# Optimization experiments

Hardware: AMD Instinct MI355X
Metric: run time of the kernel (lower is better)

Reference implementation:

```python
import jax, jax.numpy as jnp
import numpy as np

NUM_TOKENS = 4096
LATENT_DIM = 256
BETA = 0.25
TEMPERATURE = 1.0  # temp_init buffer value
EPS_TEMP = 1e-6


def setup_inputs() -> dict:
    key = jax.random.key(0)
    k1, k2 = jax.random.split(key)
    latent = jax.random.normal(k1, (4, 2048, LATENT_DIM), dtype=jnp.float32)
    cb = jax.random.normal(k2, (NUM_TOKENS, LATENT_DIM), dtype=jnp.float32)
    # module normalizes codebook rows at init
    codebook = cb / jnp.linalg.norm(cb, axis=-1, keepdims=True)
    return {"latent": latent, "codebook": codebook}


def _l2norm(x):
    return x / jnp.clip(jnp.linalg.norm(x, axis=-1, keepdims=True), 1e-12)


def reference(latent, codebook):
    B, S, D = latent.shape
    flat = latent.reshape(-1, D)                       # [N, D]
    # cosine similarity via normalized matmul
    ln = _l2norm(flat)
    cn = _l2norm(codebook)
    cosine_sim = jnp.einsum('nd,kd->nk', ln, cn)       # [N, K]
    distances = 2.0 - 2.0 * cosine_sim
    scaled = distances / jnp.maximum(TEMPERATURE, EPS_TEMP)
    soft_assign = jax.nn.softmax(-scaled, axis=-1)     # [N, K]
    indices = jnp.argmax(soft_assign, axis=-1)         # [N]
    hard_assign = jax.nn.one_hot(indices, NUM_TOKENS, dtype=jnp.float32)
    # straight-through soft->hard assignment
    assign = hard_assign + soft_assign - jax.lax.stop_gradient(soft_assign)

    selected_cosine_sim = jnp.take_along_axis(cosine_sim, indices[:, None], axis=1).mean()

    # codebook pairwise euclidean diagnostics (off-diagonal mean / min)
    sq = jnp.sum(codebook * codebook, axis=-1)         # [K]
    d2 = sq[:, None] + sq[None, :] - 2.0 * (codebook @ codebook.T)
    cdist = jnp.sqrt(jnp.clip(d2, 0.0))                # [K, K]
    K = NUM_TOKENS
    off_sum = jnp.sum(cdist) - jnp.sum(jnp.diagonal(cdist))
    avg_euclidean = off_sum / (K * (K - 1))
    eye = jnp.eye(K, dtype=bool)
    min_euclidean = jnp.min(jnp.where(eye, jnp.inf, cdist))

    quantized = (assign @ codebook).reshape(B, S, D)
    commitment_loss = BETA * jnp.mean((jax.lax.stop_gradient(latent) - quantized) ** 2)
    codebook_loss = jnp.mean((latent - jax.lax.stop_gradient(quantized)) ** 2)
    quantized = latent + jax.lax.stop_gradient(quantized - latent)

    avg_probs = jnp.mean(hard_assign, axis=0)
    perplexity = jnp.exp(-jnp.sum(avg_probs * jnp.log(avg_probs + 1e-10)))

    return (quantized, indices, commitment_loss, codebook_loss, perplexity,
            selected_cosine_sim, avg_euclidean, min_euclidean)
```

## Files before the change

### kernel.cpp

```cpp
#include <hip/hip_runtime.h>
#include <hip/hip_bf16.h>
#include <math.h>

#define NTOK 8192
#define DIM 256
#define KCB 4096
#define NCB (KCB / 128)
#define NKEY 4
#define NKROW (NCB * NKEY)
#define DELTA 0.08f
#define GTIE 2e-6
#define MAXC 16
#define NPAIRB (NCB * (NCB + 1) / 2)

typedef unsigned long long ull;
typedef unsigned short ushort;
typedef __attribute__((ext_vector_type(8))) short shortx8;
typedef __attribute__((ext_vector_type(4))) float floatx4;
typedef const __attribute__((address_space(1))) void* gas_cp;
typedef __attribute__((address_space(3))) void* las_p;

__device__ __forceinline__ unsigned f2ord(float f) {
    unsigned u = __float_as_uint(f);
    return (u & 0x80000000u) ? ~u : (u | 0x80000000u);
}
__device__ __forceinline__ float ord2f(unsigned u) {
    unsigned b = (u & 0x80000000u) ? (u & 0x7FFFFFFFu) : ~u;
    return __uint_as_float(b);
}
__device__ __forceinline__ ushort f2bf(float f) {
    unsigned u = __float_as_uint(f);
    unsigned r = u + 0x7FFFu + ((u >> 16) & 1u);
    return (ushort)(r >> 16);
}

union TileSmem {
    struct { ushort a[128][64]; ushort b[128][64]; } t;
    unsigned keys[128][40];
};

__device__ __forceinline__ void stage_tile(const ushort* __restrict__ gbase,
                                           ushort (*lds)[64], int wave, int lane,
                                           int kk) {
    int p = lane & 7;
    int rsub = lane >> 3;
    int kc = p ^ (rsub & 7);
#pragma unroll
    for (int c = 0; c < 4; ++c) {
        int j = wave * 4 + c;
        const ushort* src = gbase + (size_t)(j * 8 + rsub) * DIM + kk + kc * 8;
        __builtin_amdgcn_global_load_lds((gas_cp)src, (las_p)&lds[j * 8][0], 16, 0, 0);
    }
}
__device__ __forceinline__ shortx8 frag_read(const ushort (*lds)[64], int row,
                                             int lc) {
    return *(const shortx8*)&lds[row][(lc ^ (row & 7)) * 8];
}

__device__ __forceinline__ float np_combine(const float* racc) {
    float h0 = __fadd_rn(__fadd_rn(__fadd_rn(racc[0], racc[1]), __fadd_rn(racc[2], racc[3])),
                         __fadd_rn(__fadd_rn(racc[4], racc[5]), __fadd_rn(racc[6], racc[7])));
    float h1 = __fadd_rn(__fadd_rn(__fadd_rn(racc[8], racc[9]), __fadd_rn(racc[10], racc[11])),
                         __fadd_rn(__fadd_rn(racc[12], racc[13]), __fadd_rn(racc[14], racc[15])));
    float s = __fadd_rn(h0, h1);
    return fmaxf(sqrtf(s), 1e-12f);
}

__global__ __launch_bounds__(256) void prep(const float* __restrict__ lat,
                                            const float* __restrict__ cb,
                                            float* __restrict__ nrml,
                                            float* __restrict__ nrmc,
                                            ushort* __restrict__ latbf,
                                            ushort* __restrict__ cnbf,
                                            ushort* __restrict__ cbbf,
                                            float* __restrict__ sq,
                                            unsigned* __restrict__ counts) {
    int bid = blockIdx.x, t = threadIdx.x;
    if (bid < NTOK) {
        int n = bid;
        if (n < KCB / 256) counts[n * 256 + t] = 0u;
        const float* row = lat + (size_t)n * DIM;
        latbf[(size_t)n * DIM + t] = f2bf(row[t]);
        __shared__ float racc[16];
        if (t < 16) {
            int h = t >> 3, j = t & 7;
            const float* p = row + h * 128;
            float r = __fmul_rn(p[j], p[j]);
#pragma unroll 1
            for (int i = 8; i < 128; i += 8)
                r = __fadd_rn(r, __fmul_rn(p[i + j], p[i + j]));
            racc[t] = r;
        }
        __syncthreads();
        if (t == 0) nrml[n] = np_combine(racc);
    } else {
        int n = bid - NTOK;
        __shared__ float racc2[16];
        __shared__ double dacc[16];
        __shared__ float snrm;
        const float* row = cb + (size_t)n * DIM;
        if (t < 16) {
            int h = t >> 3, j = t & 7;
            const float* p = row + h * 128;
            float r = __fmul_rn(p[j], p[j]);
            double ds = 0.0;
#pragma unroll 1
            for (int i = 8; i < 128; i += 8)
                r = __fadd_rn(r, __fmul_rn(p[i + j], p[i + j]));
#pragma unroll 1
            for (int i = 0; i < 128; i += 8) { double v = (double)p[i + j]; ds += v * v; }
            racc2[t] = r; dacc[t] = ds;
        }
        __syncthreads();
        if (t == 0) {
            float nr = np_combine(racc2);
            snrm = nr; nrmc[n] = nr;
            double ds = 0.0;
            for (int i = 0; i < 16; ++i) ds += dacc[i];
            sq[n] = (float)ds;
        }
        __syncthreads();
        float c = row[t];
        cnbf[(size_t)n * DIM + t] = f2bf(c / snrm);
        cbbf[(size_t)n * DIM + t] = f2bf(c);
    }
}

__global__ __launch_bounds__(256) void scores_mfma(const ushort* __restrict__ A,
                                                   const ushort* __restrict__ B,
                                                   unsigned* __restrict__ keysw) {
    __shared__ TileSmem sm;
    int tid = threadIdx.x;
    int wave = tid >> 6, lane = tid & 63;
    int quad = lane >> 4, l15 = lane & 15;
    int rowBase = blockIdx.y * 128, colBase = blockIdx.x * 128;
    int wrow = wave * 32;
    floatx4 acc[2][8];
#pragma unroll
    for (int m = 0; m < 2; ++m)
#pragma unroll
        for (int n = 0; n < 8; ++n) acc[m][n] = (floatx4){0.f, 0.f, 0.f, 0.f};
    const ushort* gA = A + (size_t)rowBase * DIM;
    const ushort* gB = B + (size_t)colBase * DIM;
#pragma unroll 1
    for (int kk = 0; kk < DIM; kk += 64) {
        __syncthreads();
        stage_tile(gA, sm.t.a, wave, lane, kk);
        stage_tile(gB, sm.t.b, wave, lane, kk);
        __syncthreads();
#pragma unroll
        for (int s = 0; s < 2; ++s) {
            shortx8 af[2], bf[8];
#pragma unroll
            for (int mt = 0; mt < 2; ++mt)
                af[mt] = frag_read(sm.t.a, wrow + mt * 16 + l15, s * 4 + quad);
#pragma unroll
            for (int nt = 0; nt < 8; ++nt)
                bf[nt] = frag_read(sm.t.b, nt * 16 + l15, s * 4 + quad);
#pragma unroll
            for (int mt = 0; mt < 2; ++mt)
#pragma unroll
                for (int nt = 0; nt < 8; ++nt)
                    acc[mt][nt] = __builtin_amdgcn_mfma_f32_16x16x32_bf16(
                        af[mt], bf[nt], acc[mt][nt], 0, 0, 0);
        }
    }
    __syncthreads();
    unsigned colp[8];
#pragma unroll
    for (int nt = 0; nt < 8; ++nt)
        colp[nt] = 4095u - (unsigned)(colBase + nt * 16 + l15);
#pragma unroll
    for (int mt = 0; mt < 2; ++mt)
#pragma unroll
        for (int reg = 0; reg < 4; ++reg) {
            unsigned b1 = 0u, b2 = 0u;
#pragma unroll
            for (int nt = 0; nt < 8; ++nt) {
                unsigned key = (f2ord(acc[mt][nt][reg]) & 0xFFFFF000u) | colp[nt];
                unsigned lo = min(key, b1);
                b1 = max(key, b1);
                b2 = max(lo, b2);
            }
            int row = wrow + mt * 16 + quad * 4 + reg;
            uint2 kv; kv.x = b1; kv.y = b2;
            *(uint2*)&sm.keys[row][l15 * 2] = kv;
        }
    __syncthreads();
    if (tid < 128) {
        unsigned a0 = 0, a1 = 0, a2 = 0, a3 = 0;
#pragma unroll
        for (int j = 0; j < 8; ++j) {
            uint4 v4 = *(const uint4*)&sm.keys[tid][j * 4];
            unsigned vs[4] = {v4.x, v4.y, v4.z, v4.w};
#pragma unroll
            for (int q = 0; q < 4; ++q) {
                unsigned v = vs[q];
                unsigned n0 = min(v, a0); a0 = max(v, a0);
                unsigned n1 = min(n0, a1); a1 = max(n0, a1);
                unsigned n2 = min(n1, a2); a2 = max(n1, a2);
                a3 = max(n2, a3);
            }
        }
        size_t base = (size_t)(rowBase + tid) * NKROW + blockIdx.x * NKEY;
        uint4 o; o.x = a0; o.y = a1; o.z = a2; o.w = a3;
        *(uint4*)&keysw[base] = o;
    }
}

__global__ __launch_bounds__(256) void pairwise_mfma(const ushort* __restrict__ C,
                                                     const float* __restrict__ sq,
                                                     float* __restrict__ psumw,
                                                     unsigned* __restrict__ pminw) {
    int tri = blockIdx.x;
    int a = (int)((sqrtf(8.f * tri + 1.f) - 1.f) * 0.5f);
    while ((a + 1) * (a + 2) / 2 <= tri) ++a;
    while (a * (a + 1) / 2 > tri) --a;
    int b = tri - a * (a + 1) / 2;
    int rowBase = b * 128, colBase = a * 128;
    __shared__ TileSmem sm;
    __shared__ float rs[256], rm[256];
    int tid = threadIdx.x;
    int wave = tid >> 6, lane = tid & 63;
    int quad = lane >> 4, l15 = lane & 15;
    int wrow = wave * 32;
    floatx4 acc[2][8];
#pragma unroll
    for (int m = 0; m < 2; ++m)
#pragma unroll
        for (int n = 0; n < 8; ++n) acc[m][n] = (floatx4){0.f, 0.f, 0.f, 0.f};
    const ushort* gA = C + (size_t)rowBase * DIM;
    const ushort* gB = C + (size_t)colBase * DIM;
#pragma unroll 1
    for (int kk = 0; kk < DIM; kk += 64) {
        __syncthreads();
        stage_tile(gA, sm.t.a, wave, lane, kk);
        stage_tile(gB, sm.t.b, wave, lane, kk);
        __syncthreads();
#pragma unroll
        for (int s = 0; s < 2; ++s) {
            shortx8 af[2], bf[8];
#pragma unroll
            for (int mt = 0; mt < 2; ++mt)
                af[mt] = frag_read(sm.t.a, wrow + mt * 16 + l15, s * 4 + quad);
#pragma unroll
            for (int nt = 0; nt < 8; ++nt)
                bf[nt] = frag_read(sm.t.b, nt * 16 + l15, s * 4 + quad);
#pragma unroll
            for (int mt = 0; mt < 2; ++mt)
#pragma unroll
                for (int nt = 0; nt < 8; ++nt)
                    acc[mt][nt] = __builtin_amdgcn_mfma_f32_16x16x32_bf16(
                        af[mt], bf[nt], acc[mt][nt], 0, 0, 0);
        }
    }
    float lsum = 0.f, lmin = INFINITY;
#pragma unroll
    for (int mt = 0; mt < 2; ++mt)
#pragma unroll
        for (int reg = 0; reg < 4; ++reg) {
            int i = rowBase + wrow + mt * 16 + quad * 4 + reg;
            float sqi = sq[i];
#pragma unroll
            for (int nt = 0; nt < 8; ++nt) {
                int j = colBase + nt * 16 + l15;
                float d2 = sqi + sq[j] - 2.0f * acc[mt][nt][reg];
                float d = sqrtf(fmaxf(d2, 0.0f));
                bool use = i < j;
                lsum += use ? d : 0.f;
                lmin = fminf(lmin, use ? d : INFINITY);
            }
        }
    rs[tid] = lsum; rm[tid] = lmin; __syncthreads();
    for (int s = 128; s > 0; s >>= 1) {
        if (tid < s) { rs[tid] += rs[tid + s]; rm[tid] = fminf(rm[tid], rm[tid + s]); }
        __syncthreads();
    }
    if (tid == 0) { psumw[tri] = rs[0]; pminw[tri] = f2ord(rm[0]); }
}

__global__ __launch_bounds__(256) void argmax_resolve(const float* __restrict__ lat,
                                                      const float* __restrict__ cb,
                                                      const float* __restrict__ nrml,
                                                      const float* __restrict__ nrmc,
                                                      const unsigned* __restrict__ keysw,
                                                      float* __restrict__ outidx,
                                                      float* __restrict__ outq,
                                                      unsigned* __restrict__ counts,
                                                      float* __restrict__ selw,
                                                      float* __restrict__ msew) {
    __shared__ int scand[4][MAXC];
    __shared__ double sc64[4][MAXC];
    int wid = threadIdx.x >> 6, lane = threadIdx.x & 63;
    int n = blockIdx.x * 4 + wid;
    const unsigned* kr = keysw + (size_t)n * NKROW;
    uint2 kv = *(const uint2*)(kr + lane * 2);
    unsigned m = max(kv.x, kv.y);
#pragma unroll
    for (int off = 1; off < 64; off <<= 1) {
        unsigned o = __shfl_xor(m, off, 64);
        m = max(m, o);
    }
    float v1 = ord2f(m & 0xFFFFF000u);
    float thresh = v1 - DELTA;
    bool p0 = ord2f(kv.x & 0xFFFFF000u) >= thresh;
    bool p1 = ord2f(kv.y & 0xFFFFF000u) >= thresh;
    ull b0 = __ballot(p0), b1 = __ballot(p1);
    int below0 = __builtin_amdgcn_mbcnt_hi((unsigned)(b0 >> 32),
                 __builtin_amdgcn_mbcnt_lo((unsigned)b0, 0));
    int below1 = __builtin_amdgcn_mbcnt_hi((unsigned)(b1 >> 32),
                 __builtin_amdgcn_mbcnt_lo((unsigned)b1, 0));
    int base1 = __popcll(b0);
    int nc = base1 + __popcll(b1);
    if (p0 && below0 < MAXC)
        scand[wid][below0] = 4095 - (int)(kv.x & 0xFFFu);
    if (p1 && base1 + below1 < MAXC)
        scand[wid][base1 + below1] = 4095 - (int)(kv.y & 0xFFFu);
    nc = nc < MAXC ? nc : MAXC;
    __threadfence_block();
    float nx = nrml[n];
    int d0 = lane * 4;
    float4 xv = *(const float4*)(lat + (size_t)n * DIM + d0);
    int idx; float selcos;
    if (nc <= 1) {
        idx = 4095 - (int)(m & 0xFFFu);
        selcos = v1 / nx;
    } else {
        float la0 = xv.x / nx, la1 = xv.y / nx, la2 = xv.z / nx, la3 = xv.w / nx;
        for (int c = 0; c < nc; ++c) {
            int k = scand[wid][c];
            float nk = nrmc[k];
            float4 cv = *(const float4*)(cb + (size_t)k * DIM + d0);
            double part = (double)(cv.x / nk) * la0 + (double)(cv.y / nk) * la1 +
                          (double)(cv.z / nk) * la2 + (double)(cv.w / nk) * la3;
#pragma unroll
            for (int off = 1; off < 64; off <<= 1) part += __shfl_xor(part, off, 64);
            if (lane == 0) sc64[wid][c] = part;
        }
        __threadfence_block();
        double best64 = -1e300;
        for (int c = 0; c < nc; ++c) best64 = fmax(best64, sc64[wid][c]);
        int nrisk = 0;
        for (int c = 0; c < nc; ++c) if (sc64[wid][c] >= best64 - GTIE) ++nrisk;
        if (nrisk == 1) {
            idx = 0x7FFFFFFF; selcos = 0.f;
            for (int c = 0; c < nc; ++c)
                if (sc64[wid][c] >= best64 - GTIE) { idx = scand[wid][c]; selcos = (float)sc64[wid][c]; }
        } else {
            ull keyf = 0ull, keym = 0ull;
            if (lane < nc && sc64[wid][lane] >= best64 - GTIE) {
                int k = scand[wid][lane];
                const float* cr = cb + (size_t)k * DIM;
                const float* x = lat + (size_t)n * DIM;
                float nk = nrmc[k];
                float af = 0.f, am = 0.f;
                for (int d = 0; d < DIM; ++d) {
                    float la = x[d] / nx;
                    float cv = cr[d] / nk;
                    af = fmaf(la, cv, af);
                    am = __fadd_rn(am, __fmul_rn(la, cv));
                }
                float df = __fsub_rn(2.0f, __fmul_rn(2.0f, af));
                float dm = __fsub_rn(2.0f, __fmul_rn(2.0f, am));
                keyf = ((ull)(0xFFFFFFFFu - f2ord(df)) << 32) | (ull)(0xFFFFFFFFu - (unsigned)k);
                keym = ((ull)(0xFFFFFFFFu - f2ord(dm)) << 32) | (ull)(0xFFFFFFFFu - (unsigned)k);
            }
#pragma unroll
            for (int off = 1; off < 64; off <<= 1) {
                ull of = __shfl_xor(keyf, off, 64);
                ull om = __shfl_xor(keym, off, 64);
                keyf = of > keyf ? of : keyf;
                keym = om > keym ? om : keym;
            }
            int colf = (int)(0xFFFFFFFFu - (unsigned)(keyf & 0xFFFFFFFFull));
            int colm = (int)(0xFFFFFFFFu - (unsigned)(keym & 0xFFFFFFFFull));
            idx = colf < colm ? colf : colm;
            selcos = 0.f;
            for (int c = 0; c < nc; ++c)
                if (scand[wid][c] == idx) selcos = (float)sc64[wid][c];
        }
    }
    float4 qv = *(const float4*)(cb + (size_t)idx * DIM + d0);
    *(float4*)(outq + (size_t)n * DIM + d0) = qv;
    float dx = xv.x - qv.x, dy = xv.y - qv.y, dz = xv.z - qv.z, dw = xv.w - qv.w;
    float msep = fmaf(dx, dx, fmaf(dy, dy, fmaf(dz, dz, dw * dw)));
#pragma unroll
    for (int off = 1; off < 64; off <<= 1) msep += __shfl_xor(msep, off, 64);
    if (lane == 0) {
        outidx[n] = (float)idx;
        atomicAdd(&counts[idx], 1u);
        selw[n] = selcos;
        msew[n] = msep;
    }
}

__global__ void finalize(const unsigned* __restrict__ counts,
                         const float* __restrict__ selw,
                         const float* __restrict__ msew,
                         const float* __restrict__ psumw,
                         const unsigned* __restrict__ pminw,
                         float* __restrict__ outs) {
    int t = threadIdx.x;
    __shared__ float red[256];
    float h = 0.f;
    for (int k = t; k < KCB; k += 256) {
        float p = (float)counts[k] * (1.0f / (float)NTOK);
        h += p * logf(p + 1e-10f);
    }
    red[t] = h; __syncthreads();
    for (int s = 128; s > 0; s >>= 1) { if (t < s) red[t] += red[t + s]; __syncthreads(); }
    float entNeg = red[0];
    __syncthreads();
    float ssel = 0.f;
    for (int k = t; k < NTOK; k += 256) ssel += selw[k];
    red[t] = ssel; __syncthreads();
    for (int s = 128; s > 0; s >>= 1) { if (t < s) red[t] += red[t + s]; __syncthreads(); }
    float selSum = red[0];
    __syncthreads();
    float sm = 0.f;
    for (int k = t; k < NTOK; k += 256) sm += msew[k];
    red[t] = sm; __syncthreads();
    for (int s = 128; s > 0; s >>= 1) { if (t < s) red[t] += red[t + s]; __syncthreads(); }
    float mseSum = red[0];
    __syncthreads();
    float ps = 0.f;
    for (int k = t; k < NPAIRB; k += 256) ps += psumw[k];
    red[t] = ps; __syncthreads();
    for (int s = 128; s > 0; s >>= 1) { if (t < s) red[t] += red[t + s]; __syncthreads(); }
    float pairSum = red[0];
    __syncthreads();
    unsigned pm = 0xFFFFFFFFu;
    for (int k = t; k < NPAIRB; k += 256) pm = min(pm, pminw[k]);
    ((unsigned*)red)[t] = pm; __syncthreads();
    for (int s = 128; s > 0; s >>= 1) {
        if (t < s) ((unsigned*)red)[t] = min(((unsigned*)red)[t], ((unsigned*)red)[t + s]);
        __syncthreads();
    }
    unsigned pairMin = ((unsigned*)red)[0];
    if (t == 0) {
        float mse = mseSum / (float)(NTOK * DIM);
        outs[0] = 0.25f * mse;
        outs[1] = mse;
        outs[2] = expf(-entNeg);
        outs[3] = selSum / (float)NTOK;
        outs[4] = pairSum * 2.0f / ((float)KCB * (float)(KCB - 1));
        outs[5] = ord2f(pairMin);
    }
}

extern "C" void kernel_launch(void* const* d_in, const int* in_sizes, int n_in,
                              void* d_out, int out_size, void* d_ws, size_t ws_size,
                              hipStream_t stream) {
    const float* latent = (const float*)d_in[0];
    const float* codebook = (const float*)d_in[1];
    float* out = (float*)d_out;
    float* outq = out;
    float* outidx = out + (size_t)NTOK * DIM;
    float* outs = outidx + NTOK;

    unsigned* keysw = (unsigned*)d_ws;
    ushort* latbf = (ushort*)(keysw + (size_t)NKROW * NTOK);
    ushort* cnbf = latbf + (size_t)NTOK * DIM;
    ushort* cbbf = cnbf + (size_t)KCB * DIM;
    float* nrml = (float*)(cbbf + (size_t)KCB * DIM);
    float* nrmc = nrml + NTOK;
    float* sq = nrmc + KCB;
    unsigned* counts = (unsigned*)(sq + KCB);
    float* selw = (float*)(counts + KCB);
    float* msew = selw + NTOK;
    float* psumw = msew + NTOK;
    unsigned* pminw = (unsigned*)(psumw + NPAIRB);

    hipLaunchKernelGGL(prep, dim3(NTOK + KCB), dim3(256), 0, stream,
                       latent, codebook, nrml, nrmc, latbf, cnbf, cbbf, sq, counts);
    hipLaunchKernelGGL(scores_mfma, dim3(NCB, NTOK / 128), dim3(256), 0, stream, latbf, cnbf, keysw);
    hipLaunchKernelGGL(argmax_resolve, dim3(NTOK / 4), dim3(256), 0, stream,
                       latent, codebook, nrml, nrmc, keysw, outidx, outq, counts, selw, msew);
    hipLaunchKernelGGL(pairwise_mfma, dim3(NPAIRB), dim3(256), 0, stream, cbbf, sq, psumw, pminw);
    hipLaunchKernelGGL(finalize, dim3(1), dim3(256), 0, stream, counts, selw, msew, psumw, pminw, outs);
}
```

Before: 185.0 us.

## Merge score and pairwise GEMMs into one launch with 2-wave 64-row tiles

Combines the latent-codebook score GEMM and the codebook pairwise-distance GEMM into a single kernel whose blocks choose their role from the block index. This removes one launch and lets the two GEMMs fill the GPU together. Blocks shrink from 4 to 2 waves, each wave owning 64 rows (4x8 MFMA tiles) so every B fragment is reused across more A fragments. The cost is higher register pressure per wave and fewer waves per block to hide latency. The key scratch stride and the reduction buffers are resized to fit the shared union.

```diff
diff --git a/kernel.cpp b/kernel.cpp
--- a/kernel.cpp
+++ b/kernel.cpp
@@ -12,6 +12,7 @@
 #define GTIE 2e-6
 #define MAXC 16
 #define NPAIRB (NCB * (NCB + 1) / 2)
+#define NSCOB (NCB * (NTOK / 128))
 
 typedef unsigned long long ull;
 typedef unsigned short ushort;
@@ -36,7 +37,8 @@
 
 union TileSmem {
     struct { ushort a[128][64]; ushort b[128][64]; } t;
-    unsigned keys[128][40];
+    unsigned keys[128][33];
+    struct { float rs[128]; float rm[128]; } red;
 };
 
 __device__ __forceinline__ void stage_tile(const ushort* __restrict__ gbase,
@@ -45,11 +47,12 @@
     int p = lane & 7;
     int rsub = lane >> 3;
     int kc = p ^ (rsub & 7);
-#pragma unroll
-    for (int c = 0; c < 4; ++c) {
-        int j = wave * 4 + c;
-        const ushort* src = gbase + (size_t)(j * 8 + rsub) * DIM + kk + kc * 8;
-        __builtin_amdgcn_global_load_lds((gas_cp)src, (las_p)&lds[j * 8][0], 16, 0, 0);
+    const ushort* src0 = gbase + (size_t)(wave * 64 + rsub) * DIM + kk + kc * 8;
+#pragma unroll
+    for (int c = 0; c < 8; ++c) {
+        const ushort* src = src0 + (size_t)(c * 8) * DIM;
+        __builtin_amdgcn_global_load_lds((gas_cp)src, (las_p)&lds[wave * 64 + c * 8][0],
+                                         16, 0, 0);
     }
 }
 __device__ __forceinline__ shortx8 frag_read(const ushort (*lds)[64], int row,
@@ -126,22 +129,42 @@
     }
 }
 
-__global__ __launch_bounds__(256) void scores_mfma(const ushort* __restrict__ A,
-                                                   const ushort* __restrict__ B,
-                                                   unsigned* __restrict__ keysw) {
+__global__ __launch_bounds__(128, 2) void gemms(const ushort* __restrict__ latbf,
+                                                const ushort* __restrict__ cnbf,
+                                                const ushort* __restrict__ cbbf,
+                                                const float* __restrict__ sq,
+                                                unsigned* __restrict__ keysw,
+                                                float* __restrict__ psumw,
+                                                unsigned* __restrict__ pminw) {
     __shared__ TileSmem sm;
     int tid = threadIdx.x;
     int wave = tid >> 6, lane = tid & 63;
     int quad = lane >> 4, l15 = lane & 15;
-    int rowBase = blockIdx.y * 128, colBase = blockIdx.x * 128;
-    int wrow = wave * 32;
-    floatx4 acc[2][8];
-#pragma unroll
-    for (int m = 0; m < 2; ++m)
+    int wrow = wave * 64;
+    bool isScore = blockIdx.x < NSCOB;
+    int rowBase, colBase, tri = 0;
+    const ushort *gA, *gB;
+    if (isScore) {
+        int cbk = blockIdx.x & (NCB - 1);
+        int rbk = blockIdx.x >> 5;
+        rowBase = rbk * 128; colBase = cbk * 128;
+        gA = latbf + (size_t)rowBase * DIM;
+        gB = cnbf + (size_t)colBase * DIM;
+    } else {
+        tri = blockIdx.x - NSCOB;
+        int a = (int)((sqrtf(8.f * tri + 1.f) - 1.f) * 0.5f);
+        while ((a + 1) * (a + 2) / 2 <= tri) ++a;
+        while (a * (a + 1) / 2 > tri) --a;
+        int b = tri - a * (a + 1) / 2;
+        rowBase = b * 128; colBase = a * 128;
+        gA = cbbf + (size_t)rowBase * DIM;
+        gB = cbbf + (size_t)colBase * DIM;
+    }
+    floatx4 acc[4][8];
+#pragma unroll
+    for (int m = 0; m < 4; ++m)
 #pragma unroll
         for (int n = 0; n < 8; ++n) acc[m][n] = (floatx4){0.f, 0.f, 0.f, 0.f};
-    const ushort* gA = A + (size_t)rowBase * DIM;
-    const ushort* gB = B + (size_t)colBase * DIM;
 #pragma unroll 1
     for (int kk = 0; kk < DIM; kk += 64) {
         __syncthreads();
@@ -150,133 +173,90 @@
         __syncthreads();
 #pragma unroll
         for (int s = 0; s < 2; ++s) {
-            shortx8 af[2], bf[8];
-#pragma unroll
-            for (int mt = 0; mt < 2; ++mt)
+            shortx8 af[4];
+#pragma unroll
+            for (int mt = 0; mt < 4; ++mt)
                 af[mt] = frag_read(sm.t.a, wrow + mt * 16 + l15, s * 4 + quad);
 #pragma unroll
-            for (int nt = 0; nt < 8; ++nt)
-                bf[nt] = frag_read(sm.t.b, nt * 16 + l15, s * 4 + quad);
-#pragma unroll
-            for (int mt = 0; mt < 2; ++mt)
-#pragma unroll
-                for (int nt = 0; nt < 8; ++nt)
+            for (int nt = 0; nt < 8; ++nt) {
+                shortx8 bfr = frag_read(sm.t.b, nt * 16 + l15, s * 4 + quad);
+#pragma unroll
+                for (int mt = 0; mt < 4; ++mt)
                     acc[mt][nt] = __builtin_amdgcn_mfma_f32_16x16x32_bf16(
-                        af[mt], bf[nt], acc[mt][nt], 0, 0, 0);
+                        af[mt], bfr, acc[mt][nt], 0, 0, 0);
+            }
         }
     }
     __syncthreads();
-    unsigned colp[8];
-#pragma unroll
-    for (int nt = 0; nt < 8; ++nt)
-        colp[nt] = 4095u - (unsigned)(colBase + nt * 16 + l15);
-#pragma unroll
-    for (int mt = 0; mt < 2; ++mt)
-#pragma unroll
-        for (int reg = 0; reg < 4; ++reg) {
-            unsigned b1 = 0u, b2 = 0u;
-#pragma unroll
-            for (int nt = 0; nt < 8; ++nt) {
-                unsigned key = (f2ord(acc[mt][nt][reg]) & 0xFFFFF000u) | colp[nt];
-                unsigned lo = min(key, b1);
-                b1 = max(key, b1);
-                b2 = max(lo, b2);
-            }
-            int row = wrow + mt * 16 + quad * 4 + reg;
-            uint2 kv; kv.x = b1; kv.y = b2;
-            *(uint2*)&sm.keys[row][l15 * 2] = kv;
-        }
-    __syncthreads();
-    if (tid < 128) {
-        unsigned a0 = 0, a1 = 0, a2 = 0, a3 = 0;
-#pragma unroll
-        for (int j = 0; j < 8; ++j) {
-            uint4 v4 = *(const uint4*)&sm.keys[tid][j * 4];
-            unsigned vs[4] = {v4.x, v4.y, v4.z, v4.w};
-#pragma unroll
-            for (int q = 0; q < 4; ++q) {
-                unsigned v = vs[q];
-                unsigned n0 = min(v, a0); a0 = max(v, a0);
-                unsigned n1 = min(n0, a1); a1 = max(n0, a1);
-                unsigned n2 = min(n1, a2); a2 = max(n1, a2);
-                a3 = max(n2, a3);
-            }
-        }
-        size_t base = (size_t)(rowBase + tid) * NKROW + blockIdx.x * NKEY;
-        uint4 o; o.x = a0; o.y = a1; o.z = a2; o.w = a3;
-        *(uint4*)&keysw[base] = o;
-    }
-}
-
-__global__ __launch_bounds__(256) void pairwise_mfma(const ushort* __restrict__ C,
-                                                     const float* __restrict__ sq,
-                                                     float* __restrict__ psumw,
-                                                     unsigned* __restrict__ pminw) {
-    int tri = blockIdx.x;
-    int a = (int)((sqrtf(8.f * tri + 1.f) - 1.f) * 0.5f);
-    while ((a + 1) * (a + 2) / 2 <= tri) ++a;
-    while (a * (a + 1) / 2 > tri) --a;
-    int b = tri - a * (a + 1) / 2;
-    int rowBase = b * 128, colBase = a * 128;
-    __shared__ TileSmem sm;
-    __shared__ float rs[256], rm[256];
-    int tid = threadIdx.x;
-    int wave = tid >> 6, lane = tid & 63;
-    int quad = lane >> 4, l15 = lane & 15;
-    int wrow = wave * 32;
-    floatx4 acc[2][8];
-#pragma unroll
-    for (int m = 0; m < 2; ++m)
-#pragma unroll
-        for (int n = 0; n < 8; ++n) acc[m][n] = (floatx4){0.f, 0.f, 0.f, 0.f};
-    const ushort* gA = C + (size_t)rowBase * DIM;
-    const ushort* gB = C + (size_t)colBase * DIM;
-#pragma unroll 1
-    for (int kk = 0; kk < DIM; kk += 64) {
-        __syncthreads();
-        stage_tile(gA, sm.t.a, wave, lane, kk);
-        stage_tile(gB, sm.t.b, wave, lane, kk);
-        __syncthreads();
-#pragma unroll
-        for (int s = 0; s < 2; ++s) {
-            shortx8 af[2], bf[8];
-#pragma unroll
-            for (int mt = 0; mt < 2; ++mt)
-                af[mt] = frag_read(sm.t.a, wrow + mt * 16 + l15, s * 4 + quad);
-#pragma unroll
-            for (int nt = 0; nt < 8; ++nt)
-                bf[nt] = frag_read(sm.t.b, nt * 16 + l15, s * 4 + quad);
-#pragma unroll
-            for (int mt = 0; mt < 2; ++mt)
-#pragma unroll
-                for (int nt = 0; nt < 8; ++nt)
-                    acc[mt][nt] = __builtin_amdgcn_mfma_f32_16x16x32_bf16(
-                        af[mt], bf[nt], acc[mt][nt], 0, 0, 0);
-        }
-    }
-    float lsum = 0.f, lmin = INFINITY;
-#pragma unroll
-    for (int mt = 0; mt < 2; ++mt)
-#pragma unroll
-        for (int reg = 0; reg < 4; ++reg) {
-            int i = rowBase + wrow + mt * 16 + quad * 4 + reg;
-            float sqi = sq[i];
-#pragma unroll
-            for (int nt = 0; nt < 8; ++nt) {
-                int j = colBase + nt * 16 + l15;
-                float d2 = sqi + sq[j] - 2.0f * acc[mt][nt][reg];
-                float d = sqrtf(fmaxf(d2, 0.0f));
-                bool use = i < j;
-                lsum += use ? d : 0.f;
-                lmin = fminf(lmin, use ? d : INFINITY);
-            }
-        }
-    rs[tid] = lsum; rm[tid] = lmin; __syncthreads();
-    for (int s = 128; s > 0; s >>= 1) {
-        if (tid < s) { rs[tid] += rs[tid + s]; rm[tid] = fminf(rm[tid], rm[tid + s]); }
-        __syncthreads();
-    }
-    if (tid == 0) { psumw[tri] = rs[0]; pminw[tri] = f2ord(rm[0]); }
+    if (isScore) {
+        unsigned colp[8];
+#pragma unroll
+        for (int nt = 0; nt < 8; ++nt)
+            colp[nt] = 4095u - (unsigned)(colBase + nt * 16 + l15);
+#pragma unroll
+        for (int mt = 0; mt < 4; ++mt)
+#pragma unroll
+            for (int reg = 0; reg < 4; ++reg) {
+                unsigned b1 = 0u, b2 = 0u;
+#pragma unroll
+                for (int nt = 0; nt < 8; ++nt) {
+                    unsigned key = (f2ord(acc[mt][nt][reg]) & 0xFFFFF000u) | colp[nt];
+                    unsigned lo = min(key, b1);
+                    b1 = max(key, b1);
+                    b2 = max(lo, b2);
+                }
+                int row = wrow + mt * 16 + quad * 4 + reg;
+                uint2 kv; kv.x = b1; kv.y = b2;
+                *(uint2*)&sm.keys[row][l15 * 2] = kv;
+            }
+        __syncthreads();
+        {
+            unsigned a0 = 0, a1 = 0, a2 = 0, a3 = 0;
+#pragma unroll
+            for (int j = 0; j < 8; ++j) {
+                uint4 v4 = *(const uint4*)&sm.keys[tid][j * 4];
+                unsigned vs[4] = {v4.x, v4.y, v4.z, v4.w};
+#pragma unroll
+                for (int q = 0; q < 4; ++q) {
+                    unsigned v = vs[q];
+                    unsigned n0 = min(v, a0); a0 = max(v, a0);
+                    unsigned n1 = min(n0, a1); a1 = max(n0, a1);
+                    unsigned n2 = min(n1, a2); a2 = max(n1, a2);
+                    a3 = max(n2, a3);
+                }
+            }
+            size_t base = (size_t)(rowBase + tid) * NKROW + (blockIdx.x & (NCB - 1)) * NKEY;
+            uint4 o; o.x = a0; o.y = a1; o.z = a2; o.w = a3;
+            *(uint4*)&keysw[base] = o;
+        }
+    } else {
+        float lsum = 0.f, lmin = INFINITY;
+#pragma unroll
+        for (int mt = 0; mt < 4; ++mt)
+#pragma unroll
+            for (int reg = 0; reg < 4; ++reg) {
+                int i = rowBase + wrow + mt * 16 + quad * 4 + reg;
+                float sqi = sq[i];
+#pragma unroll
+                for (int nt = 0; nt < 8; ++nt) {
+                    int j = colBase + nt * 16 + l15;
+                    float d2 = sqi + sq[j] - 2.0f * acc[mt][nt][reg];
+                    float d = sqrtf(fmaxf(d2, 0.0f));
+                    bool use = i < j;
+                    lsum += use ? d : 0.f;
+                    lmin = fminf(lmin, use ? d : INFINITY);
+                }
+            }
+        sm.red.rs[tid] = lsum; sm.red.rm[tid] = lmin; __syncthreads();
+        for (int s = 64; s > 0; s >>= 1) {
+            if (tid < s) {
+                sm.red.rs[tid] += sm.red.rs[tid + s];
+                sm.red.rm[tid] = fminf(sm.red.rm[tid], sm.red.rm[tid + s]);
+            }
+            __syncthreads();
+        }
+        if (tid == 0) { psumw[tri] = sm.red.rs[0]; pminw[tri] = f2ord(sm.red.rm[0]); }
+    }
 }
 
 __global__ __launch_bounds__(256) void argmax_resolve(const float* __restrict__ lat,
@@ -473,9 +453,9 @@
 
     hipLaunchKernelGGL(prep, dim3(NTOK + KCB), dim3(256), 0, stream,
                        latent, codebook, nrml, nrmc, latbf, cnbf, cbbf, sq, counts);
-    hipLaunchKernelGGL(scores_mfma, dim3(NCB, NTOK / 128), dim3(256), 0, stream, latbf, cnbf, keysw);
+    hipLaunchKernelGGL(gemms, dim3(NSCOB + NPAIRB), dim3(128), 0, stream,
+                       latbf, cnbf, cbbf, sq, keysw, psumw, pminw);
     hipLaunchKernelGGL(argmax_resolve, dim3(NTOK / 4), dim3(256), 0, stream,
                        latent, codebook, nrml, nrmc, keysw, outidx, outq, counts, selw, msew);
-    hipLaunchKernelGGL(pairwise_mfma, dim3(NPAIRB), dim3(256), 0, stream, cbbf, sq, psumw, pminw);
     hipLaunchKernelGGL(finalize, dim3(1), dim3(256), 0, stream, counts, selw, msew, psumw, pminw, outs);
 }
```

New measurement: 176.2 us (median of 2 runs). 4.8% less time.
